# Optimization experiments

Measured on AMD Instinct MI355X. Metric: run time of the kernel, lower is better.

Reference implementation:

```python
import jax, jax.numpy as jnp
import numpy as np

DIM = 128; HEADS = 4; DIM_HEAD = 32; INNER = HEADS * DIM_HEAD
N = 320; B = 1
SCALE = DIM_HEAD ** -0.5


def _layernorm(x, g, b, eps=1e-5):
    mu = jnp.mean(x, -1, keepdims=True)
    var = jnp.mean((x - mu) ** 2, -1, keepdims=True)
    return (x - mu) * jax.lax.rsqrt(var + eps) * g + b


def _axial(x, row, ng, nb, wb, wq, wkv, wg, bg, wo, bo):
    # x: [B, N, N, D] pairwise repr. edges = un-normalized x (per block forward).
    xn = _layernorm(x, ng, nb)
    bias = jnp.einsum('bijd,hd->bhij', x, wb)          # [B, H, N, N] edge bias
    xt = xn if row else jnp.swapaxes(xn, 1, 2)         # [B, R, L, D], attend along L
    Bk, R, L, _ = xt.shape
    q = jnp.einsum('brld,ed->brle', xt, wq).reshape(Bk, R, L, HEADS, DIM_HEAD) * SCALE
    kv = jnp.einsum('brld,ed->brle', xt, wkv)
    k = kv[..., :INNER].reshape(Bk, R, L, HEADS, DIM_HEAD)
    v = kv[..., INNER:].reshape(Bk, R, L, HEADS, DIM_HEAD)
    # bias is shared across the folded axial dim R (torch repeat 'b h i j -> (b x) h i j')
    dots = jnp.einsum('brihe,brjhe->brhij', q, k) + bias[:, None]
    attn = jax.nn.softmax(dots, axis=-1)
    out = jnp.einsum('brhij,brjhe->brihe', attn, v).reshape(Bk, R, L, INNER)
    gates = jax.nn.sigmoid(jnp.einsum('brld,ed->brle', xt, wg) + bg)
    out = jnp.einsum('brle,de->brld', out * gates, wo) + bo
    return out if row else jnp.swapaxes(out, 1, 2)


def setup_inputs() -> dict:
    key = jax.random.key(0)
    ks = jax.random.split(key, 16)
    w = lambda k, s: jax.random.normal(k, s, jnp.float32) * 0.05
    inp = {'x': jax.random.normal(ks[0], (B, N, N, DIM), jnp.float32)}
    for i, pre in enumerate(('o_', 'i_')):
        base = 1 + 7 * i
        inp[pre + 'ng'] = jnp.ones((DIM,), jnp.float32)
        inp[pre + 'nb'] = jnp.zeros((DIM,), jnp.float32)
        inp[pre + 'wb'] = w(ks[base], (HEADS, DIM))
        inp[pre + 'wq'] = w(ks[base + 1], (INNER, DIM))
        inp[pre + 'wkv'] = w(ks[base + 2], (2 * INNER, DIM))
        inp[pre + 'wg'] = w(ks[base + 3], (INNER, DIM))
        inp[pre + 'bg'] = jnp.ones((INNER,), jnp.float32)
        inp[pre + 'wo'] = w(ks[base + 4], (DIM, INNER))
        inp[pre + 'bo'] = jnp.zeros((DIM,), jnp.float32)
    return inp


def reference(x, o_ng, o_nb, o_wb, o_wq, o_wkv, o_wg, o_bg, o_wo, o_bo,
              i_ng, i_nb, i_wb, i_wq, i_wkv, i_wg, i_bg, i_wo, i_bo):
    x = _axial(x, True, o_ng, o_nb, o_wb, o_wq, o_wkv, o_wg, o_bg, o_wo, o_bo) + x
    x = _axial(x, False, i_ng, i_nb, i_wb, i_wq, i_wkv, i_wg, i_bg, i_wo, i_bo) + x
    return x
```

## Files before the change

kernel.cpp:

```cpp
#include <hip/hip_runtime.h>
#include <hip/hip_bf16.h>

typedef unsigned short u16;
typedef unsigned int   u32;
typedef __attribute__((ext_vector_type(8))) short short8;
typedef __attribute__((ext_vector_type(4))) float f32x4;

#define NN 320
#define NP (NN*NN)
#define DD 128
#define NH 4
#define DHH 32
#define QSCALE 0.17677669529663687f
#define LOG2E  1.4426950408889634f

#define MFMA16(A,B,C) __builtin_amdgcn_mfma_f32_16x16x32_bf16(A,B,C,0,0,0)

__device__ __forceinline__ float b2f(u16 u){
    union { u32 i; float f; } v; v.i = ((u32)u) << 16; return v.f;
}
__device__ __forceinline__ u16 f2b(float f){
    union { float f; u32 i; } v; v.f = f;
    u32 x = v.i;
    u32 r = x + 0x7fffu + ((x >> 16) & 1u);
    return (u16)(r >> 16);
}
__device__ __forceinline__ u32 cvtpk(float lo, float hi){
    u32 r; asm("v_cvt_pk_bf16_f32 %0, %1, %2" : "=v"(r) : "v"(lo), "v"(hi)); return r;
}
__device__ __forceinline__ float fexp2(float x){
    float r; asm("v_exp_f32 %0, %1" : "=v"(r) : "v"(x)); return r;
}
__device__ __forceinline__ float frcp(float x){
    float r; asm("v_rcp_f32 %0, %1" : "=v"(r) : "v"(x)); return r;
}

__global__ __launch_bounds__(256) void k_pack(
    const float* w0, const float* w1, const float* w2, const float* w3, const float* w4,
    const float* w5, const float* w6, const float* w7, const float* w8, const float* w9,
    u16* __restrict__ Wp)
{
    const int m = blockIdx.x >> 3;
    const int rem = ((blockIdx.x & 7) << 8) + threadIdx.x;
    const float* src;
    switch(m){
        case 0: src=w0; break; case 1: src=w1; break; case 2: src=w2; break;
        case 3: src=w3; break; case 4: src=w4; break; case 5: src=w5; break;
        case 6: src=w6; break; case 7: src=w7; break; case 8: src=w8; break;
        default: src=w9; break;
    }
    const float4 a = *(const float4*)(src + (size_t)rem*8);
    const float4 b = *(const float4*)(src + (size_t)rem*8 + 4);
    union { uint4 q; u16 us[8]; } ww;
    ww.us[0]=f2b(a.x); ww.us[1]=f2b(a.y); ww.us[2]=f2b(a.z); ww.us[3]=f2b(a.w);
    ww.us[4]=f2b(b.x); ww.us[5]=f2b(b.y); ww.us[6]=f2b(b.z); ww.us[7]=f2b(b.w);
    const int e = rem >> 4, slot = rem & 15;
    const int dst = (e << 4) + (slot ^ (e & 15));
    *(uint4*)(Wp + ((size_t)m*2048 + dst)*8) = ww.q;
}

__global__ __launch_bounds__(256) void k_lnqkvg(
    const float* __restrict__ xin, const float* __restrict__ ng, const float* __restrict__ nb,
    const float* __restrict__ wb, const u16* __restrict__ Wp, const float* __restrict__ bg,
    float* __restrict__ biasT,
    u16* __restrict__ Pq, u16* __restrict__ Pk, u16* __restrict__ Pv, u16* __restrict__ Pg)
{
    __shared__ u16 As[128*128];
    __shared__ u16 Ws[128*128];
    const int tid = threadIdx.x;
    const int pbase = blockIdx.x * 128;
    const int s  = tid & 15;
    const int d0 = s * 8;

    const float4 g0 = *(const float4*)(ng + d0), g1 = *(const float4*)(ng + d0 + 4);
    const float4 b0 = *(const float4*)(nb + d0), b1 = *(const float4*)(nb + d0 + 4);

    #pragma unroll
    for (int c = 0; c < 8; ++c){
        const int row = (tid >> 4) + c*16;
        const int p = pbase + row;
        const float* xr = xin + (size_t)p*DD + d0;
        const float4 xa = *(const float4*)xr, xb = *(const float4*)(xr + 4);
        const float xs[8] = {xa.x,xa.y,xa.z,xa.w,xb.x,xb.y,xb.z,xb.w};
        float sum = 0.f, sq = 0.f;
        #pragma unroll
        for (int u = 0; u < 8; ++u){ sum += xs[u]; sq += xs[u]*xs[u]; }
        #pragma unroll
        for (int m = 1; m < 16; m <<= 1){
            sum += __shfl_xor(sum, m);
            sq  += __shfl_xor(sq,  m);
        }
        const float mu = sum * (1.f/128.f);
        const float var = fmaxf(sq * (1.f/128.f) - mu*mu, 0.f);
        const float rstd = rsqrtf(var + 1e-5f);
        const float gg[8] = {g0.x,g0.y,g0.z,g0.w,g1.x,g1.y,g1.z,g1.w};
        const float bbv[8]= {b0.x,b0.y,b0.z,b0.w,b1.x,b1.y,b1.z,b1.w};
        float y[8];
        #pragma unroll
        for (int u = 0; u < 8; ++u) y[u] = (xs[u]-mu)*rstd*gg[u] + bbv[u];
        uint4 o;
        o.x = cvtpk(y[0],y[1]); o.y = cvtpk(y[2],y[3]);
        o.z = cvtpk(y[4],y[5]); o.w = cvtpk(y[6],y[7]);
        *(uint4*)&As[row*128 + ((s ^ (row & 7)) << 3)] = o;

        float bh0=0.f, bh1=0.f, bh2=0.f, bh3=0.f;
        {
            const float4 wa = *(const float4*)(wb + 0*DD + d0), wbv_ = *(const float4*)(wb + 0*DD + d0 + 4);
            const float wv[8] = {wa.x,wa.y,wa.z,wa.w,wbv_.x,wbv_.y,wbv_.z,wbv_.w};
            #pragma unroll
            for (int u = 0; u < 8; ++u) bh0 += xs[u]*wv[u];
        }
        {
            const float4 wa = *(const float4*)(wb + 1*DD + d0), wbv_ = *(const float4*)(wb + 1*DD + d0 + 4);
            const float wv[8] = {wa.x,wa.y,wa.z,wa.w,wbv_.x,wbv_.y,wbv_.z,wbv_.w};
            #pragma unroll
            for (int u = 0; u < 8; ++u) bh1 += xs[u]*wv[u];
        }
        {
            const float4 wa = *(const float4*)(wb + 2*DD + d0), wbv_ = *(const float4*)(wb + 2*DD + d0 + 4);
            const float wv[8] = {wa.x,wa.y,wa.z,wa.w,wbv_.x,wbv_.y,wbv_.z,wbv_.w};
            #pragma unroll
            for (int u = 0; u < 8; ++u) bh2 += xs[u]*wv[u];
        }
        {
            const float4 wa = *(const float4*)(wb + 3*DD + d0), wbv_ = *(const float4*)(wb + 3*DD + d0 + 4);
            const float wv[8] = {wa.x,wa.y,wa.z,wa.w,wbv_.x,wbv_.y,wbv_.z,wbv_.w};
            #pragma unroll
            for (int u = 0; u < 8; ++u) bh3 += xs[u]*wv[u];
        }
        #pragma unroll
        for (int m = 1; m < 16; m <<= 1){
            bh0 += __shfl_xor(bh0, m); bh1 += __shfl_xor(bh1, m);
            bh2 += __shfl_xor(bh2, m); bh3 += __shfl_xor(bh3, m);
        }
        if (s < 4){
            const float bsel = (s == 0) ? bh0 : (s == 1) ? bh1 : (s == 2) ? bh2 : bh3;
            const int pi = p / NN, pj = p - pi*NN;
            const int it = pi >> 4, lb = pi & 15;
            const int ch = (pj >= 160) ? 1 : 0;
            const int jj = pj - ch*160;
            const int jt = jj >> 4, rr = jj & 15;
            const int gb = rr >> 2, qb = rr & 3;
            const size_t idx = (((((size_t)s*20 + it)*2 + ch)*10 + jt)*4 + gb)*64 + lb*4 + qb;
            biasT[idx] = bsel * LOG2E;
        }
    }

    const int w = tid >> 6, l = tid & 63;
    const int li = l & 15, g = l >> 4;
    const int wr = w >> 1, wc = w & 1;

    #pragma unroll
    for (int p = 0; p < 4; ++p){
        if (p > 0) __syncthreads();
        #pragma unroll
        for (int c = 0; c < 8; ++c){
            const int flat = tid + c*256;
            const uint4 wv = *(const uint4*)(Wp + ((size_t)p*2048 + flat)*8);
            *(uint4*)&Ws[flat*8] = wv;
        }
        __syncthreads();

        f32x4 acc[4][4] = {};
        #pragma unroll
        for (int ks = 0; ks < 4; ++ks){
            const int slot = ks*4 + g;
            short8 af[4];
            #pragma unroll
            for (int mt = 0; mt < 4; ++mt){
                const int row = wr*64 + mt*16 + li;
                af[mt] = *(const short8*)&As[row*128 + ((slot ^ (row & 7)) << 3)];
            }
            #pragma unroll
            for (int nt = 0; nt < 4; ++nt){
                const int e = wc*64 + nt*16 + li;
                const short8 wf = *(const short8*)&Ws[((e << 4) + (slot ^ (e & 15))) * 8];
                #pragma unroll
                for (int mt = 0; mt < 4; ++mt)
                    acc[mt][nt] = MFMA16(wf, af[mt], acc[mt][nt]);
            }
        }

        u16* Op = (p == 0) ? Pq : (p == 1) ? Pk : Pv;
        #pragma unroll
        for (int mt = 0; mt < 4; ++mt){
            const int pos = pbase + wr*64 + mt*16 + li;
            #pragma unroll
            for (int nt = 0; nt < 4; ++nt){
                const int eb = wc*64 + nt*16 + g*4;
                float v[4];
                #pragma unroll
                for (int q = 0; q < 4; ++q) v[q] = acc[mt][nt][q];
                if (p == 0){
                    #pragma unroll
                    for (int q = 0; q < 4; ++q) v[q] *= (QSCALE * LOG2E);
                } else if (p == 3){
                    #pragma unroll
                    for (int q = 0; q < 4; ++q) v[q] = frcp(1.f + fexp2(-LOG2E*(v[q] + bg[eb+q])));
                }
                uint2 o;
                o.x = cvtpk(v[0], v[1]);
                o.y = cvtpk(v[2], v[3]);
                if (p < 3){
                    u16* dst = Op + ((size_t)(eb >> 5)*NP + pos)*32 + (eb & 31);
                    *(uint2*)dst = o;
                } else {
                    *(uint2*)(Pg + (size_t)pos*DD + eb) = o;
                }
            }
        }
    }
}

__global__ __launch_bounds__(256) void k_oproj(
    const u16* __restrict__ Aatt, const u16* __restrict__ Pg, const u16* __restrict__ Wp,
    float* __restrict__ Outp, const float* __restrict__ bov, const float* __restrict__ xres)
{
    __shared__ u16 As[128*128];
    __shared__ u16 Ws[128*128];
    const int tid = threadIdx.x;
    const int pbase = blockIdx.x * 128;

    #pragma unroll
    for (int c = 0; c < 8; ++c){
        const int flat = tid + c*256;
        const int row = flat >> 4, s = flat & 15;
        const size_t off = (size_t)(pbase+row)*DD + s*8;
        union { uint4 q; u16 us[8]; } ua, ug;
        ua.q = *(const uint4*)(Aatt + off);
        ug.q = *(const uint4*)(Pg + off);
        uint4 o;
        o.x = cvtpk(b2f(ua.us[0])*b2f(ug.us[0]), b2f(ua.us[1])*b2f(ug.us[1]));
        o.y = cvtpk(b2f(ua.us[2])*b2f(ug.us[2]), b2f(ua.us[3])*b2f(ug.us[3]));
        o.z = cvtpk(b2f(ua.us[4])*b2f(ug.us[4]), b2f(ua.us[5])*b2f(ug.us[5]));
        o.w = cvtpk(b2f(ua.us[6])*b2f(ug.us[6]), b2f(ua.us[7])*b2f(ug.us[7]));
        *(uint4*)&As[row*128 + ((s ^ (row & 7)) << 3)] = o;
        const uint4 wv = *(const uint4*)(Wp + ((size_t)4*2048 + flat)*8);
        *(uint4*)&Ws[flat*8] = wv;
    }
    __syncthreads();

    const int w = tid >> 6, l = tid & 63;
    const int li = l & 15, g = l >> 4;
    const int wr = w >> 1, wc = w & 1;
    f32x4 acc[4][4] = {};

    #pragma unroll
    for (int ks = 0; ks < 4; ++ks){
        const int slot = ks*4 + g;
        short8 af[4];
        #pragma unroll
        for (int mt = 0; mt < 4; ++mt){
            const int row = wr*64 + mt*16 + li;
            af[mt] = *(const short8*)&As[row*128 + ((slot ^ (row & 7)) << 3)];
        }
        #pragma unroll
        for (int nt = 0; nt < 4; ++nt){
            const int e = wc*64 + nt*16 + li;
            const short8 wf = *(const short8*)&Ws[((e << 4) + (slot ^ (e & 15))) * 8];
            #pragma unroll
            for (int mt = 0; mt < 4; ++mt)
                acc[mt][nt] = MFMA16(wf, af[mt], acc[mt][nt]);
        }
    }

    #pragma unroll
    for (int mt = 0; mt < 4; ++mt){
        const int pos = pbase + wr*64 + mt*16 + li;
        #pragma unroll
        for (int nt = 0; nt < 4; ++nt){
            const int d0 = wc*64 + nt*16 + g*4;
            const float4 xr = *(const float4*)(xres + (size_t)pos*DD + d0);
            const float4 bo4 = *(const float4*)(bov + d0);
            float4 o;
            o.x = acc[mt][nt][0] + bo4.x + xr.x;
            o.y = acc[mt][nt][1] + bo4.y + xr.y;
            o.z = acc[mt][nt][2] + bo4.z + xr.z;
            o.w = acc[mt][nt][3] + bo4.w + xr.w;
            *(float4*)(Outp + (size_t)pos*DD + d0) = o;
        }
    }
}

template<int ROWPASS>
__global__ __launch_bounds__(256) void k_attn_mfma(
    const u16* __restrict__ Pq, const u16* __restrict__ Pk, const u16* __restrict__ Pv,
    const float* __restrict__ biasT, u16* __restrict__ Aout)
{
    __shared__ u16 ksm[320*32];
    __shared__ u16 vt[32*320];
    const int h = blockIdx.x, r = blockIdx.y;
    const int tid = threadIdx.x;

    const u16* Kh = Pk + (size_t)h*NP*32;
    const u16* Vh = Pv + (size_t)h*NP*32;
    const u16* Qh = Pq + (size_t)h*NP*32;

    #pragma unroll
    for (int c = 0; c < 5; ++c){
        const int flat = tid + c*256;
        const int j = flat >> 2, s = flat & 3;
        const size_t pos = ROWPASS ? ((size_t)r*NN + j) : ((size_t)j*NN + r);
        const uint4 k4 = *(const uint4*)(Kh + pos*32 + s*8);
        *(uint4*)&ksm[j*32 + ((s ^ ((j >> 1) & 3)) << 3)] = k4;
        const uint4 v4 = *(const uint4*)(Vh + pos*32 + s*8);
        union { uint4 q; u16 us[8]; } vu; vu.q = v4;
        const int jp = (j & ~31) + ((j >> 2) & 3)*8 + ((j >> 4) & 1)*4 + (j & 3);
        #pragma unroll
        for (int u = 0; u < 8; ++u){
            const int e = s*8 + u;
            vt[e*320 + (((jp >> 3) ^ (e & 7)) << 3) + (jp & 7)] = vu.us[u];
        }
    }
    __syncthreads();

    const int w = tid >> 6, l = tid & 63;
    const int li = l & 15, g = l >> 4;

    for (int t = 0; t < 5; ++t){
        const int it = w + t*4;
        const int i0 = it * 16;
        const int iq = i0 + li;
        const size_t qpos = ROWPASS ? ((size_t)r*NN + iq) : ((size_t)iq*NN + r);
        const short8 qf = *(const short8*)(Qh + qpos*32 + g*8);

        float mrun = -3.0e38f;
        float rsum = 0.f;
        f32x4 o0 = {0.f,0.f,0.f,0.f}, o1 = {0.f,0.f,0.f,0.f};

        #pragma unroll
        for (int ch = 0; ch < 2; ++ch){
            f32x4 st[10];
            const float* bp = biasT + ((((size_t)h*20 + it)*2 + ch)*10)*256 + g*64 + li*4;
            #pragma unroll
            for (int jt = 0; jt < 10; ++jt)
                st[jt] = *(const f32x4*)(bp + jt*256);

            #pragma unroll
            for (int jt = 0; jt < 10; ++jt){
                const int jr = ch*160 + jt*16 + li;
                const short8 kf = *(const short8*)&ksm[jr*32 + ((g ^ ((jr >> 1) & 3)) << 3)];
                st[jt] = MFMA16(kf, qf, st[jt]);
            }

            float mx = -3.0e38f;
            #pragma unroll
            for (int jt = 0; jt < 10; ++jt)
                mx = fmaxf(mx, fmaxf(fmaxf(st[jt][0], st[jt][1]), fmaxf(st[jt][2], st[jt][3])));
            mx = fmaxf(mx, __shfl_xor(mx, 16));
            mx = fmaxf(mx, __shfl_xor(mx, 32));
            const float mnew = fmaxf(mrun, mx);
            const float sc = fexp2(mrun - mnew);
            #pragma unroll
            for (int q = 0; q < 4; ++q){ o0[q] *= sc; o1[q] *= sc; }
            rsum *= sc;
            mrun = mnew;

            #pragma unroll
            for (int jt = 0; jt < 10; ++jt){
                #pragma unroll
                for (int q = 0; q < 4; ++q){
                    const float e = fexp2(st[jt][q] - mrun);
                    st[jt][q] = e; rsum += e;
                }
            }

            #pragma unroll
            for (int kt = 0; kt < 5; ++kt){
                union { u32 u[4]; short8 s8; } pu;
                pu.u[0] = cvtpk(st[2*kt][0],   st[2*kt][1]);
                pu.u[1] = cvtpk(st[2*kt][2],   st[2*kt][3]);
                pu.u[2] = cvtpk(st[2*kt+1][0], st[2*kt+1][1]);
                pu.u[3] = cvtpk(st[2*kt+1][2], st[2*kt+1][3]);
                const int ktg = ch*5 + kt;
                const int slot = ((ktg*4 + g) ^ (li & 7)) << 3;
                const short8 v0 = *(const short8*)&vt[li*320 + slot];
                const short8 v1 = *(const short8*)&vt[(16+li)*320 + slot];
                o0 = MFMA16(v0, pu.s8, o0);
                o1 = MFMA16(v1, pu.s8, o1);
            }
        }

        rsum += __shfl_xor(rsum, 16);
        rsum += __shfl_xor(rsum, 32);
        const float inv = frcp(rsum);

        u16* dst = Aout + qpos*DD + h*DHH;
        #pragma unroll
        for (int et = 0; et < 2; ++et){
            const f32x4 oo = et ? o1 : o0;
            uint2 o;
            o.x = cvtpk(oo[0]*inv, oo[1]*inv);
            o.y = cvtpk(oo[2]*inv, oo[3]*inv);
            *(uint2*)(dst + et*16 + g*4) = o;
        }
    }
}

extern "C" void kernel_launch(void* const* d_in, const int* in_sizes, int n_in,
                              void* d_out, int out_size, void* d_ws, size_t ws_size,
                              hipStream_t stream)
{
    const float* x = (const float*)d_in[0];
    float* out = (float*)d_out;
    char* ws = (char*)d_ws;

    u16*   Aatt  = (u16*)ws;
    float* biasT = (float*)(ws + (size_t)NP*DD*2);
    u16*   Pq    = (u16*)(ws + (size_t)NP*DD*2 + (size_t)NH*NP*4);
    u16*   Pk    = Pq + (size_t)NP*DD;
    u16*   Pv    = Pk + (size_t)NP*DD;
    u16*   Pg    = Pv + (size_t)NP*DD;
    u16*   Wpck  = Pg + (size_t)NP*DD;

    {
        const float* w0 = (const float*)d_in[4];
        const float* w1 = (const float*)d_in[5];
        const float* w2 = (const float*)d_in[5] + DD*DD;
        const float* w3 = (const float*)d_in[6];
        const float* w4 = (const float*)d_in[8];
        const float* w5 = (const float*)d_in[13];
        const float* w6 = (const float*)d_in[14];
        const float* w7 = (const float*)d_in[14] + DD*DD;
        const float* w8 = (const float*)d_in[15];
        const float* w9 = (const float*)d_in[17];
        k_pack<<<80, 256, 0, stream>>>(w0,w1,w2,w3,w4,w5,w6,w7,w8,w9, Wpck);
    }

    for (int pass = 0; pass < 2; ++pass){
        void* const* W = d_in + 1 + pass*9;
        const float* ng = (const float*)W[0];
        const float* nb = (const float*)W[1];
        const float* wb = (const float*)W[2];
        const float* bg = (const float*)W[6];
        const float* bo = (const float*)W[8];
        const float* xin = (pass == 0) ? x : out;
        const u16* Wp = Wpck + (size_t)pass*5*2048*8;

        k_lnqkvg<<<NP/128, 256, 0, stream>>>(xin, ng, nb, wb, Wp, bg, biasT, Pq, Pk, Pv, Pg);
        if (pass == 0) k_attn_mfma<1><<<dim3(NH, NN), 256, 0, stream>>>(Pq, Pk, Pv, biasT, Aatt);
        else           k_attn_mfma<0><<<dim3(NH, NN), 256, 0, stream>>>(Pq, Pk, Pv, biasT, Aatt);
        k_oproj<<<NP/128, 256, 0, stream>>>(Aatt, Pg, Wp, out, bo, xin);
    }
}
```

Measured before the change: 278.9 us.

## Halve weight LDS tile and store Q transposed for column pass

The weight tile in shared memory shrinks from 128x128 to 64x128. The weight pack is re-laid out into two K-halves so each GEMM stages one half at a time, which lowers LDS use per block and may allow more blocks per CU at the cost of extra barriers. In the column pass the QKV kernel also writes Q in transposed position order, so the attention kernel reads contiguous Q rows instead of strided ones. The attention kernel's output indexing is split from its Q read indexing to match.

Measured after the change: 293.0 us. 5.1% more time.

```diff
diff --git a/kernel.cpp b/kernel.cpp
--- a/kernel.cpp
+++ b/kernel.cpp
@@ -55,10 +55,12 @@
     ww.us[0]=f2b(a.x); ww.us[1]=f2b(a.y); ww.us[2]=f2b(a.z); ww.us[3]=f2b(a.w);
     ww.us[4]=f2b(b.x); ww.us[5]=f2b(b.y); ww.us[6]=f2b(b.z); ww.us[7]=f2b(b.w);
     const int e = rem >> 4, slot = rem & 15;
-    const int dst = (e << 4) + (slot ^ (e & 15));
+    const int hf = slot >> 3, s7 = slot & 7;
+    const int dst = hf*1024 + e*8 + (s7 ^ (e & 7));
     *(uint4*)(Wp + ((size_t)m*2048 + dst)*8) = ww.q;
 }
 
+template<int TRQ>
 __global__ __launch_bounds__(256) void k_lnqkvg(
     const float* __restrict__ xin, const float* __restrict__ ng, const float* __restrict__ nb,
     const float* __restrict__ wb, const u16* __restrict__ Wp, const float* __restrict__ bg,
@@ -66,7 +68,7 @@
     u16* __restrict__ Pq, u16* __restrict__ Pk, u16* __restrict__ Pv, u16* __restrict__ Pg)
 {
     __shared__ u16 As[128*128];
-    __shared__ u16 Ws[128*128];
+    __shared__ u16 Ws[64*128];
     const int tid = threadIdx.x;
     const int pbase = blockIdx.x * 128;
     const int s  = tid & 15;
@@ -105,26 +107,26 @@
 
         float bh0=0.f, bh1=0.f, bh2=0.f, bh3=0.f;
         {
-            const float4 wa = *(const float4*)(wb + 0*DD + d0), wbv_ = *(const float4*)(wb + 0*DD + d0 + 4);
-            const float wv[8] = {wa.x,wa.y,wa.z,wa.w,wbv_.x,wbv_.y,wbv_.z,wbv_.w};
+            const float4 wa = *(const float4*)(wb + 0*DD + d0), wv2 = *(const float4*)(wb + 0*DD + d0 + 4);
+            const float wv[8] = {wa.x,wa.y,wa.z,wa.w,wv2.x,wv2.y,wv2.z,wv2.w};
             #pragma unroll
             for (int u = 0; u < 8; ++u) bh0 += xs[u]*wv[u];
         }
         {
-            const float4 wa = *(const float4*)(wb + 1*DD + d0), wbv_ = *(const float4*)(wb + 1*DD + d0 + 4);
-            const float wv[8] = {wa.x,wa.y,wa.z,wa.w,wbv_.x,wbv_.y,wbv_.z,wbv_.w};
+            const float4 wa = *(const float4*)(wb + 1*DD + d0), wv2 = *(const float4*)(wb + 1*DD + d0 + 4);
+            const float wv[8] = {wa.x,wa.y,wa.z,wa.w,wv2.x,wv2.y,wv2.z,wv2.w};
             #pragma unroll
             for (int u = 0; u < 8; ++u) bh1 += xs[u]*wv[u];
         }
         {
-            const float4 wa = *(const float4*)(wb + 2*DD + d0), wbv_ = *(const float4*)(wb + 2*DD + d0 + 4);
-            const float wv[8] = {wa.x,wa.y,wa.z,wa.w,wbv_.x,wbv_.y,wbv_.z,wbv_.w};
+            const float4 wa = *(const float4*)(wb + 2*DD + d0), wv2 = *(const float4*)(wb + 2*DD + d0 + 4);
+            const float wv[8] = {wa.x,wa.y,wa.z,wa.w,wv2.x,wv2.y,wv2.z,wv2.w};
             #pragma unroll
             for (int u = 0; u < 8; ++u) bh2 += xs[u]*wv[u];
         }
         {
-            const float4 wa = *(const float4*)(wb + 3*DD + d0), wbv_ = *(const float4*)(wb + 3*DD + d0 + 4);
-            const float wv[8] = {wa.x,wa.y,wa.z,wa.w,wbv_.x,wbv_.y,wbv_.z,wbv_.w};
+            const float4 wa = *(const float4*)(wb + 3*DD + d0), wv2 = *(const float4*)(wb + 3*DD + d0 + 4);
+            const float wv[8] = {wa.x,wa.y,wa.z,wa.w,wv2.x,wv2.y,wv2.z,wv2.w};
             #pragma unroll
             for (int u = 0; u < 8; ++u) bh3 += xs[u]*wv[u];
         }
@@ -152,32 +154,35 @@
 
     #pragma unroll
     for (int p = 0; p < 4; ++p){
-        if (p > 0) __syncthreads();
-        #pragma unroll
-        for (int c = 0; c < 8; ++c){
-            const int flat = tid + c*256;
-            const uint4 wv = *(const uint4*)(Wp + ((size_t)p*2048 + flat)*8);
-            *(uint4*)&Ws[flat*8] = wv;
-        }
-        __syncthreads();
-
         f32x4 acc[4][4] = {};
         #pragma unroll
-        for (int ks = 0; ks < 4; ++ks){
-            const int slot = ks*4 + g;
-            short8 af[4];
-            #pragma unroll
-            for (int mt = 0; mt < 4; ++mt){
-                const int row = wr*64 + mt*16 + li;
-                af[mt] = *(const short8*)&As[row*128 + ((slot ^ (row & 7)) << 3)];
-            }
-            #pragma unroll
-            for (int nt = 0; nt < 4; ++nt){
-                const int e = wc*64 + nt*16 + li;
-                const short8 wf = *(const short8*)&Ws[((e << 4) + (slot ^ (e & 15))) * 8];
+        for (int hf = 0; hf < 2; ++hf){
+            __syncthreads();
+            #pragma unroll
+            for (int c = 0; c < 4; ++c){
+                const int flat = tid + c*256;
+                const uint4 wv = *(const uint4*)(Wp + ((size_t)p*2048 + hf*1024 + flat)*8);
+                *(uint4*)&Ws[flat*8] = wv;
+            }
+            __syncthreads();
+
+            #pragma unroll
+            for (int ks = hf*2; ks < hf*2 + 2; ++ks){
+                const int slot = ks*4 + g;
+                short8 af[4];
                 #pragma unroll
-                for (int mt = 0; mt < 4; ++mt)
-                    acc[mt][nt] = MFMA16(wf, af[mt], acc[mt][nt]);
+                for (int mt = 0; mt < 4; ++mt){
+                    const int row = wr*64 + mt*16 + li;
+                    af[mt] = *(const short8*)&As[row*128 + ((slot ^ (row & 7)) << 3)];
+                }
+                #pragma unroll
+                for (int nt = 0; nt < 4; ++nt){
+                    const int e = wc*64 + nt*16 + li;
+                    const short8 wf = *(const short8*)&Ws[((e << 3) + ((slot & 7) ^ (e & 7))) * 8];
+                    #pragma unroll
+                    for (int mt = 0; mt < 4; ++mt)
+                        acc[mt][nt] = MFMA16(wf, af[mt], acc[mt][nt]);
+                }
             }
         }
 
@@ -185,6 +190,11 @@
         #pragma unroll
         for (int mt = 0; mt < 4; ++mt){
             const int pos = pbase + wr*64 + mt*16 + li;
+            int pos_q = pos;
+            if (TRQ && p == 0){
+                const int pi = pos / NN, pj = pos - pi*NN;
+                pos_q = pj*NN + pi;
+            }
             #pragma unroll
             for (int nt = 0; nt < 4; ++nt){
                 const int eb = wc*64 + nt*16 + g*4;
@@ -202,7 +212,8 @@
                 o.x = cvtpk(v[0], v[1]);
                 o.y = cvtpk(v[2], v[3]);
                 if (p < 3){
-                    u16* dst = Op + ((size_t)(eb >> 5)*NP + pos)*32 + (eb & 31);
+                    const int ps = (p == 0) ? pos_q : pos;
+                    u16* dst = Op + ((size_t)(eb >> 5)*NP + ps)*32 + (eb & 31);
                     *(uint2*)dst = o;
                 } else {
                     *(uint2*)(Pg + (size_t)pos*DD + eb) = o;
@@ -217,7 +228,7 @@
     float* __restrict__ Outp, const float* __restrict__ bov, const float* __restrict__ xres)
 {
     __shared__ u16 As[128*128];
-    __shared__ u16 Ws[128*128];
+    __shared__ u16 Ws[64*128];
     const int tid = threadIdx.x;
     const int pbase = blockIdx.x * 128;
 
@@ -235,10 +246,7 @@
         o.z = cvtpk(b2f(ua.us[4])*b2f(ug.us[4]), b2f(ua.us[5])*b2f(ug.us[5]));
         o.w = cvtpk(b2f(ua.us[6])*b2f(ug.us[6]), b2f(ua.us[7])*b2f(ug.us[7]));
         *(uint4*)&As[row*128 + ((s ^ (row & 7)) << 3)] = o;
-        const uint4 wv = *(const uint4*)(Wp + ((size_t)4*2048 + flat)*8);
-        *(uint4*)&Ws[flat*8] = wv;
-    }
-    __syncthreads();
+    }
 
     const int w = tid >> 6, l = tid & 63;
     const int li = l & 15, g = l >> 4;
@@ -246,21 +254,33 @@
     f32x4 acc[4][4] = {};
 
     #pragma unroll
-    for (int ks = 0; ks < 4; ++ks){
-        const int slot = ks*4 + g;
-        short8 af[4];
-        #pragma unroll
-        for (int mt = 0; mt < 4; ++mt){
-            const int row = wr*64 + mt*16 + li;
-            af[mt] = *(const short8*)&As[row*128 + ((slot ^ (row & 7)) << 3)];
-        }
-        #pragma unroll
-        for (int nt = 0; nt < 4; ++nt){
-            const int e = wc*64 + nt*16 + li;
-            const short8 wf = *(const short8*)&Ws[((e << 4) + (slot ^ (e & 15))) * 8];
-            #pragma unroll
-            for (int mt = 0; mt < 4; ++mt)
-                acc[mt][nt] = MFMA16(wf, af[mt], acc[mt][nt]);
+    for (int hf = 0; hf < 2; ++hf){
+        if (hf) __syncthreads();
+        #pragma unroll
+        for (int c = 0; c < 4; ++c){
+            const int flat = tid + c*256;
+            const uint4 wv = *(const uint4*)(Wp + ((size_t)4*2048 + hf*1024 + flat)*8);
+            *(uint4*)&Ws[flat*8] = wv;
+        }
+        __syncthreads();
+
+        #pragma unroll
+        for (int ks = hf*2; ks < hf*2 + 2; ++ks){
+            const int slot = ks*4 + g;
+            short8 af[4];
+            #pragma unroll
+            for (int mt = 0; mt < 4; ++mt){
+                const int row = wr*64 + mt*16 + li;
+                af[mt] = *(const short8*)&As[row*128 + ((slot ^ (row & 7)) << 3)];
+            }
+            #pragma unroll
+            for (int nt = 0; nt < 4; ++nt){
+                const int e = wc*64 + nt*16 + li;
+                const short8 wf = *(const short8*)&Ws[((e << 3) + ((slot & 7) ^ (e & 7))) * 8];
+                #pragma unroll
+                for (int mt = 0; mt < 4; ++mt)
+                    acc[mt][nt] = MFMA16(wf, af[mt], acc[mt][nt]);
+            }
         }
     }
 
@@ -321,8 +341,8 @@
         const int it = w + t*4;
         const int i0 = it * 16;
         const int iq = i0 + li;
-        const size_t qpos = ROWPASS ? ((size_t)r*NN + iq) : ((size_t)iq*NN + r);
-        const short8 qf = *(const short8*)(Qh + qpos*32 + g*8);
+        const size_t qpos_out = ROWPASS ? ((size_t)r*NN + iq) : ((size_t)iq*NN + r);
+        const short8 qf = *(const short8*)(Qh + ((size_t)r*NN + iq)*32 + g*8);
 
         float mrun = -3.0e38f;
         float rsum = 0.f;
@@ -385,7 +405,7 @@
         rsum += __shfl_xor(rsum, 32);
         const float inv = frcp(rsum);
 
-        u16* dst = Aout + qpos*DD + h*DHH;
+        u16* dst = Aout + qpos_out*DD + h*DHH;
         #pragma unroll
         for (int et = 0; et < 2; ++et){
             const f32x4 oo = et ? o1 : o0;
@@ -437,9 +457,13 @@
         const float* xin = (pass == 0) ? x : out;
         const u16* Wp = Wpck + (size_t)pass*5*2048*8;
 
-        k_lnqkvg<<<NP/128, 256, 0, stream>>>(xin, ng, nb, wb, Wp, bg, biasT, Pq, Pk, Pv, Pg);
-        if (pass == 0) k_attn_mfma<1><<<dim3(NH, NN), 256, 0, stream>>>(Pq, Pk, Pv, biasT, Aatt);
-        else           k_attn_mfma<0><<<dim3(NH, NN), 256, 0, stream>>>(Pq, Pk, Pv, biasT, Aatt);
+        if (pass == 0){
+            k_lnqkvg<0><<<NP/128, 256, 0, stream>>>(xin, ng, nb, wb, Wp, bg, biasT, Pq, Pk, Pv, Pg);
+            k_attn_mfma<1><<<dim3(NH, NN), 256, 0, stream>>>(Pq, Pk, Pv, biasT, Aatt);
+        } else {
+            k_lnqkvg<1><<<NP/128, 256, 0, stream>>>(xin, ng, nb, wb, Wp, bg, biasT, Pq, Pk, Pv, Pg);
+            k_attn_mfma<0><<<dim3(NH, NN), 256, 0, stream>>>(Pq, Pk, Pv, biasT, Aatt);
+        }
         k_oproj<<<NP/128, 256, 0, stream>>>(Aatt, Pg, Wp, out, bo, xin);
     }
 }
```

## Store Q/K/V/gate/attn in 4-channel-group planar layout, pretranspose Q for column pass

Applied to the files above, without the earlier changes.

Switches the intermediate Q, K, V, gate and attention-output buffers from per-head 32-wide rows to a planar layout of 4-element channel groups, each group holding all positions contiguously. For the column pass, Q is written already transposed so each attention block reads its queries from contiguous positions. The aim is more coalesced global accesses in the strided column-attention pass. The cost is that every consumer now assembles 8-element fragments from two separate 8-byte loads in different planes, which may reduce per-load efficiency in the row pass and in the output projection.

After: 318.5 us. 1.14x slower.

```diff
diff --git a/kernel.cpp b/kernel.cpp
--- a/kernel.cpp
+++ b/kernel.cpp
@@ -59,6 +59,7 @@
     *(uint4*)(Wp + ((size_t)m*2048 + dst)*8) = ww.q;
 }
 
+template<int TRQ>
 __global__ __launch_bounds__(256) void k_lnqkvg(
     const float* __restrict__ xin, const float* __restrict__ ng, const float* __restrict__ nb,
     const float* __restrict__ wb, const u16* __restrict__ Wp, const float* __restrict__ bg,
@@ -105,26 +106,26 @@
 
         float bh0=0.f, bh1=0.f, bh2=0.f, bh3=0.f;
         {
-            const float4 wa = *(const float4*)(wb + 0*DD + d0), wbv_ = *(const float4*)(wb + 0*DD + d0 + 4);
-            const float wv[8] = {wa.x,wa.y,wa.z,wa.w,wbv_.x,wbv_.y,wbv_.z,wbv_.w};
+            const float4 wa = *(const float4*)(wb + 0*DD + d0), wv2 = *(const float4*)(wb + 0*DD + d0 + 4);
+            const float wv[8] = {wa.x,wa.y,wa.z,wa.w,wv2.x,wv2.y,wv2.z,wv2.w};
             #pragma unroll
             for (int u = 0; u < 8; ++u) bh0 += xs[u]*wv[u];
         }
         {
-            const float4 wa = *(const float4*)(wb + 1*DD + d0), wbv_ = *(const float4*)(wb + 1*DD + d0 + 4);
-            const float wv[8] = {wa.x,wa.y,wa.z,wa.w,wbv_.x,wbv_.y,wbv_.z,wbv_.w};
+            const float4 wa = *(const float4*)(wb + 1*DD + d0), wv2 = *(const float4*)(wb + 1*DD + d0 + 4);
+            const float wv[8] = {wa.x,wa.y,wa.z,wa.w,wv2.x,wv2.y,wv2.z,wv2.w};
             #pragma unroll
             for (int u = 0; u < 8; ++u) bh1 += xs[u]*wv[u];
         }
         {
-            const float4 wa = *(const float4*)(wb + 2*DD + d0), wbv_ = *(const float4*)(wb + 2*DD + d0 + 4);
-            const float wv[8] = {wa.x,wa.y,wa.z,wa.w,wbv_.x,wbv_.y,wbv_.z,wbv_.w};
+            const float4 wa = *(const float4*)(wb + 2*DD + d0), wv2 = *(const float4*)(wb + 2*DD + d0 + 4);
+            const float wv[8] = {wa.x,wa.y,wa.z,wa.w,wv2.x,wv2.y,wv2.z,wv2.w};
             #pragma unroll
             for (int u = 0; u < 8; ++u) bh2 += xs[u]*wv[u];
         }
         {
-            const float4 wa = *(const float4*)(wb + 3*DD + d0), wbv_ = *(const float4*)(wb + 3*DD + d0 + 4);
-            const float wv[8] = {wa.x,wa.y,wa.z,wa.w,wbv_.x,wbv_.y,wbv_.z,wbv_.w};
+            const float4 wa = *(const float4*)(wb + 3*DD + d0), wv2 = *(const float4*)(wb + 3*DD + d0 + 4);
+            const float wv[8] = {wa.x,wa.y,wa.z,wa.w,wv2.x,wv2.y,wv2.z,wv2.w};
             #pragma unroll
             for (int u = 0; u < 8; ++u) bh3 += xs[u]*wv[u];
         }
@@ -181,13 +182,19 @@
             }
         }
 
-        u16* Op = (p == 0) ? Pq : (p == 1) ? Pk : Pv;
+        u16* Op = (p == 0) ? Pq : (p == 1) ? Pk : (p == 2) ? Pv : Pg;
         #pragma unroll
         for (int mt = 0; mt < 4; ++mt){
             const int pos = pbase + wr*64 + mt*16 + li;
+            int ps = pos;
+            if (TRQ && p == 0){
+                const int pi = pos / NN, pj = pos - pi*NN;
+                ps = pj*NN + pi;
+            }
             #pragma unroll
             for (int nt = 0; nt < 4; ++nt){
                 const int eb = wc*64 + nt*16 + g*4;
+                const int eg = eb >> 2;
                 float v[4];
                 #pragma unroll
                 for (int q = 0; q < 4; ++q) v[q] = acc[mt][nt][q];
@@ -201,12 +208,7 @@
                 uint2 o;
                 o.x = cvtpk(v[0], v[1]);
                 o.y = cvtpk(v[2], v[3]);
-                if (p < 3){
-                    u16* dst = Op + ((size_t)(eb >> 5)*NP + pos)*32 + (eb & 31);
-                    *(uint2*)dst = o;
-                } else {
-                    *(uint2*)(Pg + (size_t)pos*DD + eb) = o;
-                }
+                *(uint2*)(Op + ((size_t)eg*NP + ps)*4) = o;
             }
         }
     }
@@ -225,10 +227,14 @@
     for (int c = 0; c < 8; ++c){
         const int flat = tid + c*256;
         const int row = flat >> 4, s = flat & 15;
-        const size_t off = (size_t)(pbase+row)*DD + s*8;
+        const int pos = pbase + row;
+        const uint2 a1 = *(const uint2*)(Aatt + ((size_t)(2*s)  *NP + pos)*4);
+        const uint2 a2 = *(const uint2*)(Aatt + ((size_t)(2*s+1)*NP + pos)*4);
+        const uint2 p1 = *(const uint2*)(Pg   + ((size_t)(2*s)  *NP + pos)*4);
+        const uint2 p2 = *(const uint2*)(Pg   + ((size_t)(2*s+1)*NP + pos)*4);
         union { uint4 q; u16 us[8]; } ua, ug;
-        ua.q = *(const uint4*)(Aatt + off);
-        ug.q = *(const uint4*)(Pg + off);
+        ua.q = make_uint4(a1.x, a1.y, a2.x, a2.y);
+        ug.q = make_uint4(p1.x, p1.y, p2.x, p2.y);
         uint4 o;
         o.x = cvtpk(b2f(ua.us[0])*b2f(ug.us[0]), b2f(ua.us[1])*b2f(ug.us[1]));
         o.y = cvtpk(b2f(ua.us[2])*b2f(ug.us[2]), b2f(ua.us[3])*b2f(ug.us[3]));
@@ -301,10 +307,13 @@
         const int flat = tid + c*256;
         const int j = flat >> 2, s = flat & 3;
         const size_t pos = ROWPASS ? ((size_t)r*NN + j) : ((size_t)j*NN + r);
-        const uint4 k4 = *(const uint4*)(Kh + pos*32 + s*8);
+        const uint2 ka = *(const uint2*)(Kh + ((size_t)(2*s)  *NP + pos)*4);
+        const uint2 kb = *(const uint2*)(Kh + ((size_t)(2*s+1)*NP + pos)*4);
+        const uint4 k4 = make_uint4(ka.x, ka.y, kb.x, kb.y);
         *(uint4*)&ksm[j*32 + ((s ^ ((j >> 1) & 3)) << 3)] = k4;
-        const uint4 v4 = *(const uint4*)(Vh + pos*32 + s*8);
-        union { uint4 q; u16 us[8]; } vu; vu.q = v4;
+        const uint2 va = *(const uint2*)(Vh + ((size_t)(2*s)  *NP + pos)*4);
+        const uint2 vb = *(const uint2*)(Vh + ((size_t)(2*s+1)*NP + pos)*4);
+        union { uint4 q; u16 us[8]; } vu; vu.q = make_uint4(va.x, va.y, vb.x, vb.y);
         const int jp = (j & ~31) + ((j >> 2) & 3)*8 + ((j >> 4) & 1)*4 + (j & 3);
         #pragma unroll
         for (int u = 0; u < 8; ++u){
@@ -321,8 +330,12 @@
         const int it = w + t*4;
         const int i0 = it * 16;
         const int iq = i0 + li;
-        const size_t qpos = ROWPASS ? ((size_t)r*NN + iq) : ((size_t)iq*NN + r);
-        const short8 qf = *(const short8*)(Qh + qpos*32 + g*8);
+        const size_t qpos_out = ROWPASS ? ((size_t)r*NN + iq) : ((size_t)iq*NN + r);
+        const size_t qrow = (size_t)r*NN + iq;
+        const uint2 qa = *(const uint2*)(Qh + ((size_t)(2*g)  *NP + qrow)*4);
+        const uint2 qb = *(const uint2*)(Qh + ((size_t)(2*g+1)*NP + qrow)*4);
+        union { uint4 q; short8 s8; } qfu; qfu.q = make_uint4(qa.x, qa.y, qb.x, qb.y);
+        const short8 qf = qfu.s8;
 
         float mrun = -3.0e38f;
         float rsum = 0.f;
@@ -385,14 +398,13 @@
         rsum += __shfl_xor(rsum, 32);
         const float inv = frcp(rsum);
 
-        u16* dst = Aout + qpos*DD + h*DHH;
         #pragma unroll
         for (int et = 0; et < 2; ++et){
             const f32x4 oo = et ? o1 : o0;
             uint2 o;
             o.x = cvtpk(oo[0]*inv, oo[1]*inv);
             o.y = cvtpk(oo[2]*inv, oo[3]*inv);
-            *(uint2*)(dst + et*16 + g*4) = o;
+            *(uint2*)(Aout + ((size_t)(h*8 + et*4 + g)*NP + qpos_out)*4) = o;
         }
     }
 }
@@ -437,9 +449,13 @@
         const float* xin = (pass == 0) ? x : out;
         const u16* Wp = Wpck + (size_t)pass*5*2048*8;
 
-        k_lnqkvg<<<NP/128, 256, 0, stream>>>(xin, ng, nb, wb, Wp, bg, biasT, Pq, Pk, Pv, Pg);
-        if (pass == 0) k_attn_mfma<1><<<dim3(NH, NN), 256, 0, stream>>>(Pq, Pk, Pv, biasT, Aatt);
-        else           k_attn_mfma<0><<<dim3(NH, NN), 256, 0, stream>>>(Pq, Pk, Pv, biasT, Aatt);
+        if (pass == 0){
+            k_lnqkvg<0><<<NP/128, 256, 0, stream>>>(xin, ng, nb, wb, Wp, bg, biasT, Pq, Pk, Pv, Pg);
+            k_attn_mfma<1><<<dim3(NH, NN), 256, 0, stream>>>(Pq, Pk, Pv, biasT, Aatt);
+        } else {
+            k_lnqkvg<1><<<NP/128, 256, 0, stream>>>(xin, ng, nb, wb, Wp, bg, biasT, Pq, Pk, Pv, Pg);
+            k_attn_mfma<0><<<dim3(NH, NN), 256, 0, stream>>>(Pq, Pk, Pv, biasT, Aatt);
+        }
         k_oproj<<<NP/128, 256, 0, stream>>>(Aatt, Pg, Wp, out, bo, xin);
     }
 }
```

## Store column-pass Q/K/V transposed and keep edge bias in bf16

Applied to the files above, without the earlier changes.

In the column pass, the QKV projection kernel now writes Q, K and V at transposed positions. The attention kernel can then read its K/V rows and Q vectors contiguously instead of with a stride of NN*32 elements. The precomputed edge bias is also stored as bf16 instead of fp32, which halves its memory traffic and is widened back to float on load. The costs are scattered writes in the projection epilogue, extra rounding error in the bias, and a small fix so the gate pointer expression covers all four projections.

Result: slower. 389.2 us (+39.6%).

```diff
diff --git a/kernel.cpp b/kernel.cpp
--- a/kernel.cpp
+++ b/kernel.cpp
@@ -59,10 +59,11 @@
     *(uint4*)(Wp + ((size_t)m*2048 + dst)*8) = ww.q;
 }
 
+template<int TRP>
 __global__ __launch_bounds__(256) void k_lnqkvg(
     const float* __restrict__ xin, const float* __restrict__ ng, const float* __restrict__ nb,
     const float* __restrict__ wb, const u16* __restrict__ Wp, const float* __restrict__ bg,
-    float* __restrict__ biasT,
+    u16* __restrict__ biasB,
     u16* __restrict__ Pq, u16* __restrict__ Pk, u16* __restrict__ Pv, u16* __restrict__ Pg)
 {
     __shared__ u16 As[128*128];
@@ -105,26 +106,26 @@
 
         float bh0=0.f, bh1=0.f, bh2=0.f, bh3=0.f;
         {
-            const float4 wa = *(const float4*)(wb + 0*DD + d0), wbv_ = *(const float4*)(wb + 0*DD + d0 + 4);
-            const float wv[8] = {wa.x,wa.y,wa.z,wa.w,wbv_.x,wbv_.y,wbv_.z,wbv_.w};
+            const float4 wa = *(const float4*)(wb + 0*DD + d0), wv2 = *(const float4*)(wb + 0*DD + d0 + 4);
+            const float wv[8] = {wa.x,wa.y,wa.z,wa.w,wv2.x,wv2.y,wv2.z,wv2.w};
             #pragma unroll
             for (int u = 0; u < 8; ++u) bh0 += xs[u]*wv[u];
         }
         {
-            const float4 wa = *(const float4*)(wb + 1*DD + d0), wbv_ = *(const float4*)(wb + 1*DD + d0 + 4);
-            const float wv[8] = {wa.x,wa.y,wa.z,wa.w,wbv_.x,wbv_.y,wbv_.z,wbv_.w};
+            const float4 wa = *(const float4*)(wb + 1*DD + d0), wv2 = *(const float4*)(wb + 1*DD + d0 + 4);
+            const float wv[8] = {wa.x,wa.y,wa.z,wa.w,wv2.x,wv2.y,wv2.z,wv2.w};
             #pragma unroll
             for (int u = 0; u < 8; ++u) bh1 += xs[u]*wv[u];
         }
         {
-            const float4 wa = *(const float4*)(wb + 2*DD + d0), wbv_ = *(const float4*)(wb + 2*DD + d0 + 4);
-            const float wv[8] = {wa.x,wa.y,wa.z,wa.w,wbv_.x,wbv_.y,wbv_.z,wbv_.w};
+            const float4 wa = *(const float4*)(wb + 2*DD + d0), wv2 = *(const float4*)(wb + 2*DD + d0 + 4);
+            const float wv[8] = {wa.x,wa.y,wa.z,wa.w,wv2.x,wv2.y,wv2.z,wv2.w};
             #pragma unroll
             for (int u = 0; u < 8; ++u) bh2 += xs[u]*wv[u];
         }
         {
-            const float4 wa = *(const float4*)(wb + 3*DD + d0), wbv_ = *(const float4*)(wb + 3*DD + d0 + 4);
-            const float wv[8] = {wa.x,wa.y,wa.z,wa.w,wbv_.x,wbv_.y,wbv_.z,wbv_.w};
+            const float4 wa = *(const float4*)(wb + 3*DD + d0), wv2 = *(const float4*)(wb + 3*DD + d0 + 4);
+            const float wv[8] = {wa.x,wa.y,wa.z,wa.w,wv2.x,wv2.y,wv2.z,wv2.w};
             #pragma unroll
             for (int u = 0; u < 8; ++u) bh3 += xs[u]*wv[u];
         }
@@ -142,7 +143,7 @@
             const int jt = jj >> 4, rr = jj & 15;
             const int gb = rr >> 2, qb = rr & 3;
             const size_t idx = (((((size_t)s*20 + it)*2 + ch)*10 + jt)*4 + gb)*64 + lb*4 + qb;
-            biasT[idx] = bsel * LOG2E;
+            biasB[idx] = f2b(bsel * LOG2E);
         }
     }
 
@@ -181,10 +182,15 @@
             }
         }
 
-        u16* Op = (p == 0) ? Pq : (p == 1) ? Pk : Pv;
+        u16* Op = (p == 0) ? Pq : (p == 1) ? Pk : (p == 2) ? Pv : Pg;
         #pragma unroll
         for (int mt = 0; mt < 4; ++mt){
             const int pos = pbase + wr*64 + mt*16 + li;
+            int ps = pos;
+            if (TRP && p < 3){
+                const int pi = pos / NN, pj = pos - pi*NN;
+                ps = pj*NN + pi;
+            }
             #pragma unroll
             for (int nt = 0; nt < 4; ++nt){
                 const int eb = wc*64 + nt*16 + g*4;
@@ -202,7 +208,7 @@
                 o.x = cvtpk(v[0], v[1]);
                 o.y = cvtpk(v[2], v[3]);
                 if (p < 3){
-                    u16* dst = Op + ((size_t)(eb >> 5)*NP + pos)*32 + (eb & 31);
+                    u16* dst = Op + ((size_t)(eb >> 5)*NP + ps)*32 + (eb & 31);
                     *(uint2*)dst = o;
                 } else {
                     *(uint2*)(Pg + (size_t)pos*DD + eb) = o;
@@ -285,7 +291,7 @@
 template<int ROWPASS>
 __global__ __launch_bounds__(256) void k_attn_mfma(
     const u16* __restrict__ Pq, const u16* __restrict__ Pk, const u16* __restrict__ Pv,
-    const float* __restrict__ biasT, u16* __restrict__ Aout)
+    const u16* __restrict__ biasB, u16* __restrict__ Aout)
 {
     __shared__ u16 ksm[320*32];
     __shared__ u16 vt[32*320];
@@ -300,7 +306,7 @@
     for (int c = 0; c < 5; ++c){
         const int flat = tid + c*256;
         const int j = flat >> 2, s = flat & 3;
-        const size_t pos = ROWPASS ? ((size_t)r*NN + j) : ((size_t)j*NN + r);
+        const size_t pos = (size_t)r*NN + j;
         const uint4 k4 = *(const uint4*)(Kh + pos*32 + s*8);
         *(uint4*)&ksm[j*32 + ((s ^ ((j >> 1) & 3)) << 3)] = k4;
         const uint4 v4 = *(const uint4*)(Vh + pos*32 + s*8);
@@ -321,8 +327,8 @@
         const int it = w + t*4;
         const int i0 = it * 16;
         const int iq = i0 + li;
-        const size_t qpos = ROWPASS ? ((size_t)r*NN + iq) : ((size_t)iq*NN + r);
-        const short8 qf = *(const short8*)(Qh + qpos*32 + g*8);
+        const size_t qpos_out = ROWPASS ? ((size_t)r*NN + iq) : ((size_t)iq*NN + r);
+        const short8 qf = *(const short8*)(Qh + ((size_t)r*NN + iq)*32 + g*8);
 
         float mrun = -3.0e38f;
         float rsum = 0.f;
@@ -331,10 +337,14 @@
         #pragma unroll
         for (int ch = 0; ch < 2; ++ch){
             f32x4 st[10];
-            const float* bp = biasT + ((((size_t)h*20 + it)*2 + ch)*10)*256 + g*64 + li*4;
-            #pragma unroll
-            for (int jt = 0; jt < 10; ++jt)
-                st[jt] = *(const f32x4*)(bp + jt*256);
+            const u16* bpb = biasB + ((((size_t)h*20 + it)*2 + ch)*10)*256 + g*64 + li*4;
+            #pragma unroll
+            for (int jt = 0; jt < 10; ++jt){
+                union { uint2 v; u16 us[4]; } bu;
+                bu.v = *(const uint2*)(bpb + jt*256);
+                st[jt][0] = b2f(bu.us[0]); st[jt][1] = b2f(bu.us[1]);
+                st[jt][2] = b2f(bu.us[2]); st[jt][3] = b2f(bu.us[3]);
+            }
 
             #pragma unroll
             for (int jt = 0; jt < 10; ++jt){
@@ -385,7 +395,7 @@
         rsum += __shfl_xor(rsum, 32);
         const float inv = frcp(rsum);
 
-        u16* dst = Aout + qpos*DD + h*DHH;
+        u16* dst = Aout + qpos_out*DD + h*DHH;
         #pragma unroll
         for (int et = 0; et < 2; ++et){
             const f32x4 oo = et ? o1 : o0;
@@ -406,8 +416,8 @@
     char* ws = (char*)d_ws;
 
     u16*   Aatt  = (u16*)ws;
-    float* biasT = (float*)(ws + (size_t)NP*DD*2);
-    u16*   Pq    = (u16*)(ws + (size_t)NP*DD*2 + (size_t)NH*NP*4);
+    u16*   biasB = (u16*)(ws + (size_t)NP*DD*2);
+    u16*   Pq    = (u16*)(ws + (size_t)NP*DD*2 + (size_t)NH*NP*2);
     u16*   Pk    = Pq + (size_t)NP*DD;
     u16*   Pv    = Pk + (size_t)NP*DD;
     u16*   Pg    = Pv + (size_t)NP*DD;
@@ -437,9 +447,13 @@
         const float* xin = (pass == 0) ? x : out;
         const u16* Wp = Wpck + (size_t)pass*5*2048*8;
 
-        k_lnqkvg<<<NP/128, 256, 0, stream>>>(xin, ng, nb, wb, Wp, bg, biasT, Pq, Pk, Pv, Pg);
-        if (pass == 0) k_attn_mfma<1><<<dim3(NH, NN), 256, 0, stream>>>(Pq, Pk, Pv, biasT, Aatt);
-        else           k_attn_mfma<0><<<dim3(NH, NN), 256, 0, stream>>>(Pq, Pk, Pv, biasT, Aatt);
+        if (pass == 0){
+            k_lnqkvg<0><<<NP/128, 256, 0, stream>>>(xin, ng, nb, wb, Wp, bg, biasB, Pq, Pk, Pv, Pg);
+            k_attn_mfma<1><<<dim3(NH, NN), 256, 0, stream>>>(Pq, Pk, Pv, biasB, Aatt);
+        } else {
+            k_lnqkvg<1><<<NP/128, 256, 0, stream>>>(xin, ng, nb, wb, Wp, bg, biasB, Pq, Pk, Pv, Pg);
+            k_attn_mfma<0><<<dim3(NH, NN), 256, 0, stream>>>(Pq, Pk, Pv, biasB, Aatt);
+        }
         k_oproj<<<NP/128, 256, 0, stream>>>(Aatt, Pg, Wp, out, bo, xin);
     }
 }
```
